# Kernel optimization log

Hardware: AMD Instinct MI355X
Metric: run time of the kernel (lower is better)

Reference implementation:

```python
import jax, jax.numpy as jnp
import numpy as np

B, N, D, H, E, FF = 4, 256, 256, 8, 32, 512
DK = D // H
SCALE = DK ** -0.5
NEG = -9.0e15


def _norm_mul(t, w, b, ms):
    # graph norm over node axis (dim=1)
    mean = jnp.mean(t, axis=1, keepdims=True)
    std = jnp.sqrt(jnp.mean((t - ms * mean) ** 2, axis=1, keepdims=True))
    return w * (t - ms * mean) / (std + 1e-6) + b


def _layer_norm(t, w, b):
    mu = jnp.mean(t, axis=-1, keepdims=True)
    var = jnp.mean((t - mu) ** 2, axis=-1, keepdims=True)
    return w * (t - mu) * jax.lax.rsqrt(var + 1e-5) + b


def _ffn(t, W1, b1, W2, b2):
    return jax.nn.gelu(t @ W1 + b1, approximate=False) @ W2 + b2


def _forward(x, edge_fea, attn_bias, params, adj, adj1, use_adj):
    (gn1_w, gn1_b, gn1_ms, ln1_w, ln1_b, Wq, bq, Wk, bk, Wv, bv,
     Wap, bap, Wep, bep, Wo, bo, Woe, gn2_w, gn2_b, gn2_ms,
     W1, b1, W2, b2, ln2_w, ln2_b, W1e, b1e, W2e, b2e) = params
    adj_f = adj.astype(x.dtype)
    adj1_f = adj1.astype(x.dtype)

    y = _norm_mul(x, gn1_w, gn1_b, gn1_ms)              # [B,N,D]
    e_n = _layer_norm(edge_fea, ln1_w, ln1_b)           # [B,N,N,E]

    q = (y @ Wq + bq).reshape(B, N, H, DK) * SCALE
    k = (y @ Wk + bk).reshape(B, N, H, DK)
    v = (y @ Wv + bv).reshape(B, N, H, DK)
    scores = jnp.einsum('bihd,bjhd->bhij', q, k)        # [B,H,N,N]
    if use_adj:
        scores = jnp.where(adj_f[:, None] > 0, scores, NEG) * adj_f[:, None]

    # global branch: multiplicative attn_bias then softmax
    x_long = jax.nn.softmax(scores * attn_bias, axis=-1)
    out_long = jnp.einsum('bhij,bjhd->bihd', x_long, v)

    # edge-feature fusion
    edge_bias = jnp.swapaxes(e_n @ Wep + bep, 1, 3)     # [B,H,N,N]
    x_proj = (jnp.swapaxes(scores, 1, 3) @ Wap + bap) * adj1_f[..., None]  # [B,N,N,E]
    e_attn = (e_n + x_proj) @ Woe                       # [B,N,N,E]

    # local branch: scores gated by edge bias and local adjacency
    x_local = jax.nn.softmax(scores * edge_bias * adj1_f[:, None], axis=-1)
    out_local = jnp.einsum('bhij,bjhd->bihd', x_local, v)

    attn_out = (out_local + out_long).reshape(B, N, D) @ Wo + bo

    x_out = x + attn_out
    x_out = x_out + _ffn(_norm_mul(x_out, gn2_w, gn2_b, gn2_ms), W1, b1, W2, b2)

    e1 = edge_fea + e_attn
    e_out = e1 + _ffn(_layer_norm(e1, ln2_w, ln2_b), W1e, b1e, W2e, b2e)
    return x_out, e_out


def setup_inputs() -> dict:
    key = jax.random.key(0)
    keys = list(jax.random.split(key, 32))

    def nk():
        return keys.pop()

    def w(shape, s=0.02):
        return jax.random.normal(nk(), shape, jnp.float32) * s

    inp = {}
    inp['x'] = jax.random.normal(nk(), (B, N, D), jnp.float32)
    inp['adj'] = jax.random.randint(nk(), (B, N, N), 0, 2).astype(jnp.int32)
    inp['adj1'] = (jax.random.uniform(nk(), (B, N, N)) < 0.15).astype(jnp.int32)
    inp['use_adj'] = 1
    inp['edge_fea'] = jax.random.normal(nk(), (B, N, N, E), jnp.float32)
    inp['attn_bias'] = jax.random.uniform(nk(), (B, H, N, N), jnp.float32)
    for nm, dim in [('gn1', D), ('gn2', D)]:
        inp[nm + '_w'] = jnp.ones((dim,), jnp.float32)
        inp[nm + '_b'] = jnp.zeros((dim,), jnp.float32)
        inp[nm + '_ms'] = jnp.ones((dim,), jnp.float32)
    for nm, dim in [('ln1', E), ('ln2', E)]:
        inp[nm + '_w'] = jnp.ones((dim,), jnp.float32)
        inp[nm + '_b'] = jnp.zeros((dim,), jnp.float32)
    inp['Wq'], inp['bq'] = w((D, D)), jnp.zeros((D,), jnp.float32)
    inp['Wk'], inp['bk'] = w((D, D)), jnp.zeros((D,), jnp.float32)
    inp['Wv'], inp['bv'] = w((D, D)), jnp.zeros((D,), jnp.float32)
    inp['Wap'], inp['bap'] = w((H, E)), jnp.zeros((E,), jnp.float32)
    inp['Wep'], inp['bep'] = w((E, H)), jnp.zeros((H,), jnp.float32)
    inp['Wo'], inp['bo'] = w((D, D)), jnp.zeros((D,), jnp.float32)
    inp['Woe'] = w((E, E))
    inp['W1'], inp['b1'] = w((D, FF)), jnp.zeros((FF,), jnp.float32)
    inp['W2'], inp['b2'] = w((FF, D)), jnp.zeros((D,), jnp.float32)
    inp['W1e'], inp['b1e'] = w((E, FF)), jnp.zeros((FF,), jnp.float32)
    inp['W2e'], inp['b2e'] = w((FF, E)), jnp.zeros((E,), jnp.float32)
    return inp


def reference(x, adj, adj1, use_adj, edge_fea, attn_bias,
              gn1_w, gn1_b, gn1_ms, gn2_w, gn2_b, gn2_ms,
              ln1_w, ln1_b, ln2_w, ln2_b,
              Wq, bq, Wk, bk, Wv, bv, Wap, bap, Wep, bep, Wo, bo, Woe,
              W1, b1, W2, b2, W1e, b1e, W2e, b2e):
    params = (gn1_w, gn1_b, gn1_ms, ln1_w, ln1_b, Wq, bq, Wk, bk, Wv, bv,
              Wap, bap, Wep, bep, Wo, bo, Woe, gn2_w, gn2_b, gn2_ms,
              W1, b1, W2, b2, ln2_w, ln2_b, W1e, b1e, W2e, b2e)
    return _forward(x, edge_fea, attn_bias, params, adj, adj1, use_adj)
```

## Files before the change

kernel.cpp:

```cpp
#include <hip/hip_runtime.h>
#include <math.h>

constexpr int B_ = 4, N_ = 256, D_ = 256, H_ = 8, E_ = 32, FF_ = 512, DK_ = 32;
constexpr float SCALE_ = 0.17677669529663687f;
constexpr float NEG_ = -9.0e15f;

typedef unsigned short u16;
typedef unsigned int u32;
typedef __attribute__((ext_vector_type(8))) short bf16x8;
typedef __attribute__((ext_vector_type(4))) float f32x4;
typedef __attribute__((ext_vector_type(8))) _Float16 f16x8;
typedef __attribute__((ext_vector_type(2))) _Float16 f16x2;
typedef __attribute__((ext_vector_type(2))) __fp16 fp16x2_raw;

__device__ __forceinline__ float gelu_fast(float x) {
  float u = x * x;
  float q = x * fmaf(-0.071354816272f, u, -1.5957691216057308f);
  float e = __expf(q);
  return x * __builtin_amdgcn_rcpf(1.f + e);
}

__device__ __forceinline__ f16x2 cvt_pk_f16(float a, float b) {
  union { fp16x2_raw i; f16x2 o; } u;
  u.i = __builtin_amdgcn_cvt_pkrtz(a, b);
// ... 288 lines not shown
    if (GELU) v = gelu_fast(v);
    if (res) v += res[(size_t)row * Nn + col];
    C[(size_t)row * Nn + col] = v;
  }
}

__global__ __launch_bounds__(256) void qkv_mfma_kernel(
    const float* __restrict__ A, const u16* __restrict__ wxp,
    const float* __restrict__ bq, const float* __restrict__ bk,
    const float* __restrict__ bv,
    float* __restrict__ q, float* __restrict__ k, float* __restrict__ v) {
  int z = blockIdx.z;
  const u16* Wp = wxp + (size_t)z * 65536;
  const float* bias = (z == 0) ? bq : (z == 1) ? bk : bv;
  float* C = (z == 0) ? q : (z == 1) ? k : v;
  float scale = (z == 0) ? SCALE_ : 1.f;
  int tid = threadIdx.x;
  int w = tid >> 6, l = tid & 63;
  int rt = w & 1, cts = (w >> 1) << 1;
  int row0 = blockIdx.y * 32, col0 = blockIdx.x * 64;
  f32x4 acc[2];
#pragma unroll
  for (int c2 = 0; c2 < 2; c2++) {
    float bb = bias[col0 + (cts + c2) * 16 + (l & 15)];
    acc[c2] = (f32x4){bb, bb, bb, bb};
  }
  int arow = row0 + rt * 16 + (l & 15);
  const float* ap = A + (size_t)arow * D_ + ((l >> 4) << 3);
#pragma unroll
  for (int kc = 0; kc < 8; kc++) {
    float4 a0 = *(const float4*)(ap + kc * 32);
    float4 a1 = *(const float4*)(ap + kc * 32 + 4);
    union { bf16x8 v; u32 u[4]; } af;
    af.u[0] = pk2bf(a0.x, a0.y); af.u[1] = pk2bf(a0.z, a0.w);
    af.u[2] = pk2bf(a1.x, a1.y); af.u[3] = pk2bf(a1.z, a1.w);
#pragma unroll
    for (int c2 = 0; c2 < 2; c2++) {
      bf16x8 wf = *(const bf16x8*)(Wp + (((size_t)kc * 16 + (col0 >> 4) + cts + c2) << 9) + (l << 3));
      acc[c2] = __builtin_amdgcn_mfma_f32_16x16x32_bf16(af.v, wf, acc[c2], 0, 0, 0);
    }
  }
#pragma unroll
  for (int c2 = 0; c2 < 2; c2++) {
    int col = col0 + (cts + c2) * 16 + (l & 15);
#pragma unroll
    for (int rr = 0; rr < 4; rr++) {
      int row = row0 + rt * 16 + (l >> 4) * 4 + rr;
      C[(size_t)row * D_ + col] = acc[c2][rr] * scale;
    }
  }
}

__global__ __launch_bounds__(256) void scores_attn_kernel(
    const float* __restrict__ q, const float* __restrict__ k,
    const float* __restrict__ v, const int* __restrict__ adj,
    const int* __restrict__ use_adj, const float* __restrict__ ab,
    const u16* __restrict__ eb16,
    u16* __restrict__ scoresT, float* __restrict__ out) {
  int it2 = blockIdx.x, h = blockIdx.y, b = blockIdx.z;
  int tid = threadIdx.x;
  __shared__ float qt[16][33];
  __shared__ u16 sc[16][260];
  __shared__ float vst[32][260];
  __shared__ float psw[4][256];

  float kreg[32];
  {
    const float4* kp = (const float4*)(k + ((size_t)b * N_ + tid) * D_ + h * DK_);
#pragma unroll
    for (int i = 0; i < 8; i++) {
      float4 kv = kp[i];
      kreg[4 * i] = kv.x; kreg[4 * i + 1] = kv.y;
      kreg[4 * i + 2] = kv.z; kreg[4 * i + 3] = kv.w;
    }
  }
  for (int i2 = 0; i2 < 2; i2++) {
    int f = tid + (i2 << 8);
    int rr = f >> 5, d = f & 31;
    qt[rr][d] = q[((size_t)b * N_ + it2 * 16 + rr) * D_ + h * DK_ + d];
  }
  for (int i2 = 0; i2 < 32; i2++) {
    int f = tid + (i2 << 8);
    int j = f >> 5, d = f & 31;
    vst[d][j] = v[((size_t)b * N_ + j) * D_ + h * DK_ + d];
  }
  __syncthreads();

  int ua = use_adj[0];
  u32 sbuf[8];
  float sprev = 0.f;
#pragma unroll
  for (int r = 0; r < 16; r++) {
    float s = 0.f;
#pragma unroll
    for (int d = 0; d < 32; d++) s = fmaf(qt[r][d], kreg[d], s);
    int i = it2 * 16 + r;
    if (ua) {
      int a = adj[((size_t)b * N_ + i) * N_ + tid];
      s = (a > 0 ? s : NEG_) * (float)a;
    }
    sc[r][tid] = f2bf(s);
    if (r & 1) sbuf[r >> 1] = pk2bf(sprev, s); else sprev = s;
  }
  uint4* stp = (uint4*)(scoresT + ((((size_t)(b * N_ + tid)) * 8 + h) << 8) + (it2 << 4));
  stp[0] = make_uint4(sbuf[0], sbuf[1], sbuf[2], sbuf[3]);
  stp[1] = make_uint4(sbuf[4], sbuf[5], sbuf[6], sbuf[7]);
  __syncthreads();

  int w = tid >> 6, l = tid & 63;
  int d = l & 31, hf = l >> 5;
  for (int rr = 0; rr < 4; rr++) {
    int lr = w * 4 + rr;
    int i = it2 * 16 + lr;
    size_t base = (((size_t)b * H_ + h) * N_ + i) * N_ + l * 4;
    uint2 sB = *(const uint2*)&sc[lr][l * 4];
    float s4x = bf2f((u16)(sB.x & 0xffff)), s4y = bf2f((u16)(sB.x >> 16));
    float s4z = bf2f((u16)(sB.y & 0xffff)), s4w = bf2f((u16)(sB.y >> 16));
    uint2 eB = *(const uint2*)(eb16 + base);
    float e4x = bf2f((u16)(eB.x & 0xffff)), e4y = bf2f((u16)(eB.x >> 16));
    float e4z = bf2f((u16)(eB.y & 0xffff)), e4w = bf2f((u16)(eB.y >> 16));
    float4 a4 = *(const float4*)(ab + base);
    float sl[4] = {s4x * a4.x, s4y * a4.y, s4z * a4.z, s4w * a4.w};
    float scv[4] = {s4x * e4x, s4y * e4y, s4z * e4z, s4w * e4w};
    float ml = fmaxf(fmaxf(sl[0], sl[1]), fmaxf(sl[2], sl[3]));
    float mc = fmaxf(fmaxf(scv[0], scv[1]), fmaxf(scv[2], scv[3]));
#pragma unroll
    for (int o = 32; o; o >>= 1) { ml = fmaxf(ml, __shfl_xor(ml, o)); mc = fmaxf(mc, __shfl_xor(mc, o)); }
    float el[4], ec[4];
#pragma unroll
    for (int c = 0; c < 4; c++) { el[c] = __expf(sl[c] - ml); ec[c] = __expf(scv[c] - mc); }
    float suml = el[0] + el[1] + el[2] + el[3];
    float sumc = ec[0] + ec[1] + ec[2] + ec[3];
#pragma unroll
    for (int o = 32; o; o >>= 1) { suml += __shfl_xor(suml, o); sumc += __shfl_xor(sumc, o); }
    float rl = __builtin_amdgcn_rcpf(suml), rc = __builtin_amdgcn_rcpf(sumc);
    float4 p;
    p.x = el[0] * rl + ec[0] * rc; p.y = el[1] * rl + ec[1] * rc;
    p.z = el[2] * rl + ec[2] * rc; p.w = el[3] * rl + ec[3] * rc;
    *(float4*)&psw[w][l * 4] = p;
    float acc = 0.f;
#pragma unroll
    for (int jq = 0; jq < 32; jq++) {
      int j4 = hf * 128 + jq * 4;
      float4 pp = *(const float4*)&psw[w][j4];
      float4 vv = *(const float4*)&vst[d][j4];
      acc = fmaf(pp.x, vv.x, acc); acc = fmaf(pp.y, vv.y, acc);
      acc = fmaf(pp.z, vv.z, acc); acc = fmaf(pp.w, vv.w, acc);
    }
    acc += __shfl_xor(acc, 32);
    if (l < 32) out[((size_t)b * N_ + i) * D_ + h * DK_ + d] = acc;
  }
}

__global__ __launch_bounds__(256) void e_fused_kernel(
    const u16* __restrict__ e_nb, const u16* __restrict__ scoresT,
    const int* __restrict__ adj1, const u16* __restrict__ wwp,
    const float* __restrict__ edge_fea,
    const u16* __restrict__ woep, const float* __restrict__ lw,
    const float* __restrict__ lb, const u16* __restrict__ w1p,
    const float* __restrict__ b1e, const u16* __restrict__ w2p,
    const float* __restrict__ b2e, float* __restrict__ e_out) {
  __shared__ float e1s[4][32][36];
  __shared__ float stats[4][2][32];
  int tid = threadIdx.x;
  int w = tid >> 6, l = tid & 63;
  size_t row0 = (size_t)blockIdx.x * 128 + (size_t)w * 32;
  int kb = (l >> 4) * 8;

  bf16x8 wf0 = *(const bf16x8*)(woep + l * 8);
  bf16x8 wf1 = *(const bf16x8*)(woep + 512 + l * 8);
  bf16x8 wwf0 = *(const bf16x8*)(wwp + l * 8);
  bf16x8 wwf1 = *(const bf16x8*)(wwp + 512 + l * 8);
  f32x4 zero = (f32x4){0.f, 0.f, 0.f, 0.f};
  f32x4 eo[2][2];
#pragma unroll
  for (int rt = 0; rt < 2; rt++) {
    size_t gr = row0 + rt * 16 + (l & 15);
    int a1 = adj1[gr];
    bf16x8 enf = *(const bf16x8*)(e_nb + gr * 32 + kb);
    bf16x8 sf = (bf16x8){0, 0, 0, 0, 0, 0, 0, 0};
    int kg = l >> 4;
    if (kg == 0) {
      const u16* sp = scoresT + ((size_t)(gr >> 8) * 8) * 256 + (gr & 255);
#pragma unroll
      for (int hh = 0; hh < 8; hh++)
        sf[hh] = a1 ? (short)sp[hh * 256] : (short)0;
    } else if (kg == 1) {
      sf[0] = a1 ? (short)0x3F80 : (short)0;
    }
    f32x4 acc0 = __builtin_amdgcn_mfma_f32_16x16x32_bf16(sf, wwf0, zero, 0, 0, 0);
    f32x4 acc1 = __builtin_amdgcn_mfma_f32_16x16x32_bf16(sf, wwf1, zero, 0, 0, 0);
    eo[rt][0] = __builtin_amdgcn_mfma_f32_16x16x32_bf16(enf, wf0, acc0, 0, 0, 0);
    eo[rt][1] = __builtin_amdgcn_mfma_f32_16x16x32_bf16(enf, wf1, acc1, 0, 0, 0);
  }
#pragma unroll
  for (int rt = 0; rt < 2; rt++)
#pragma unroll
    for (int ct = 0; ct < 2; ct++) {
      int col = ct * 16 + (l & 15);
#pragma unroll
      for (int rr = 0; rr < 4; rr++) {
        int row = rt * 16 + (l >> 4) * 4 + rr;
        float ed = edge_fea[(row0 + row) * E_ + col];
        e1s[w][row][col] = ed + eo[rt][ct][rr];
      }
    }

  {
    int r = l >> 1, ch = (l & 1) * 16;
    float4 v0 = *(const float4*)&e1s[w][r][ch + 0];
    float4 v1 = *(const float4*)&e1s[w][r][ch + 4];
    float4 v2 = *(const float4*)&e1s[w][r][ch + 8];
    float4 v3 = *(const float4*)&e1s[w][r][ch + 12];
    float s = v0.x + v0.y + v0.z + v0.w + v1.x + v1.y + v1.z + v1.w +
              v2.x + v2.y + v2.z + v2.w + v3.x + v3.y + v3.z + v3.w;
    s += __shfl_xor(s, 1);
    float mu = s * (1.f / E_);
    float tmp[16] = {v0.x, v0.y, v0.z, v0.w, v1.x, v1.y, v1.z, v1.w,
                     v2.x, v2.y, v2.z, v2.w, v3.x, v3.y, v3.z, v3.w};
    float q = 0.f;
#pragma unroll
    for (int i = 0; i < 16; i++) { float dd = tmp[i] - mu; q += dd * dd; }
    q += __shfl_xor(q, 1);
    float inv = rsqrtf(q * (1.f / E_) + 1e-5f);
    stats[w][0][r] = mu;
    stats[w][1][r] = inv;
  }

  bf16x8 at[2];
  {
    float4 lw0 = *(const float4*)(lw + kb), lw1 = *(const float4*)(lw + kb + 4);
    float4 lb0 = *(const float4*)(lb + kb), lb1 = *(const float4*)(lb + kb + 4);
    float lwv[8] = {lw0.x, lw0.y, lw0.z, lw0.w, lw1.x, lw1.y, lw1.z, lw1.w};
    float lbv[8] = {lb0.x, lb0.y, lb0.z, lb0.w, lb1.x, lb1.y, lb1.z, lb1.w};
#pragma unroll
    for (int rt = 0; rt < 2; rt++) {
      int ar = rt * 16 + (l & 15);
      float mu = stats[w][0][ar], inv = stats[w][1][ar];
      float4 e0 = *(const float4*)&e1s[w][ar][kb];
      float4 e1v = *(const float4*)&e1s[w][ar][kb + 4];
      float ev[8] = {e0.x, e0.y, e0.z, e0.w, e1v.x, e1v.y, e1v.z, e1v.w};
#pragma unroll
      for (int j = 0; j < 8; j++)
        at[rt][j] = (short)f2bf(lwv[j] * (ev[j] - mu) * inv + lbv[j]);
    }
  }

  f32x4 oacc[2][2];
#pragma unroll
  for (int ct = 0; ct < 2; ct++) {
    float bb = b2e[ct * 16 + (l & 15)];
#pragma unroll
    for (int rt = 0; rt < 2; rt++)
      oacc[rt][ct] = (f32x4){bb, bb, bb, bb};
  }

#pragma unroll 4
  for (int st = 0; st < 16; st++) {
    bf16x8 w1f0 = *(const bf16x8*)(w1p + (((size_t)st * 2 + 0) << 9) + (l << 3));
    bf16x8 w1f1 = *(const bf16x8*)(w1p + (((size_t)st * 2 + 1) << 9) + (l << 3));
    f16x8 w2f0 = *(const f16x8*)(w2p + (((size_t)st * 2 + 0) << 9) + (l << 3));
    f16x8 w2f1 = *(const f16x8*)(w2p + (((size_t)st * 2 + 1) << 9) + (l << 3));
    float4 b40 = *(const float4*)(b1e + st * 32 + ((l >> 4) << 2));
    float4 b41 = *(const float4*)(b1e + st * 32 + 16 + ((l >> 4) << 2));
    f32x4 hi0 = (f32x4){b40.x, b40.y, b40.z, b40.w};
    f32x4 hi1 = (f32x4){b41.x, b41.y, b41.z, b41.w};
    f32x4 ht00 = __builtin_amdgcn_mfma_f32_16x16x32_bf16(w1f0, at[0], hi0, 0, 0, 0);
    f32x4 ht01 = __builtin_amdgcn_mfma_f32_16x16x32_bf16(w1f0, at[1], hi0, 0, 0, 0);
    f32x4 ht10 = __builtin_amdgcn_mfma_f32_16x16x32_bf16(w1f1, at[0], hi1, 0, 0, 0);
    f32x4 ht11 = __builtin_amdgcn_mfma_f32_16x16x32_bf16(w1f1, at[1], hi1, 0, 0, 0);
    {
      union { f16x8 v; f16x2 h2[4]; } a8;
      a8.h2[0] = gelu_pk(cvt_pk_f16(ht00[0], ht00[1]));
      a8.h2[1] = gelu_pk(cvt_pk_f16(ht00[2], ht00[3]));
      a8.h2[2] = gelu_pk(cvt_pk_f16(ht10[0], ht10[1]));
      a8.h2[3] = gelu_pk(cvt_pk_f16(ht10[2], ht10[3]));
      oacc[0][0] = __builtin_amdgcn_mfma_f32_16x16x32_f16(a8.v, w2f0, oacc[0][0], 0, 0, 0);
      oacc[0][1] = __builtin_amdgcn_mfma_f32_16x16x32_f16(a8.v, w2f1, oacc[0][1], 0, 0, 0);
    }
    {
      union { f16x8 v; f16x2 h2[4]; } a8;
      a8.h2[0] = gelu_pk(cvt_pk_f16(ht01[0], ht01[1]));
      a8.h2[1] = gelu_pk(cvt_pk_f16(ht01[2], ht01[3]));
      a8.h2[2] = gelu_pk(cvt_pk_f16(ht11[0], ht11[1]));
      a8.h2[3] = gelu_pk(cvt_pk_f16(ht11[2], ht11[3]));
      oacc[1][0] = __builtin_amdgcn_mfma_f32_16x16x32_f16(a8.v, w2f0, oacc[1][0], 0, 0, 0);
      oacc[1][1] = __builtin_amdgcn_mfma_f32_16x16x32_f16(a8.v, w2f1, oacc[1][1], 0, 0, 0);
    }
  }

#pragma unroll
  for (int rt = 0; rt < 2; rt++)
#pragma unroll
    for (int ct = 0; ct < 2; ct++) {
      int col = ct * 16 + (l & 15);
#pragma unroll
      for (int r = 0; r < 4; r++) {
        int rl = rt * 16 + (l >> 4) * 4 + r;
        e_out[(row0 + rl) * E_ + col] = e1s[w][rl][col] + oacc[rt][ct][r];
      }
    }
}

extern "C" void kernel_launch(void* const* d_in, const int* in_sizes, int n_in,
                              void* d_out, int out_size, void* d_ws, size_t ws_size,
                              hipStream_t stream) {
  (void)in_sizes; (void)n_in; (void)out_size; (void)ws_size;
  const float* x        = (const float*)d_in[0];
  const int*   adj      = (const int*)d_in[1];
  const int*   adj1     = (const int*)d_in[2];
  const int*   use_adj  = (const int*)d_in[3];
  const float* edge_fea = (const float*)d_in[4];
  const float* attnb    = (const float*)d_in[5];
  const float* gn1_w = (const float*)d_in[6];
  const float* gn1_b = (const float*)d_in[7];
  const float* gn1_ms = (const float*)d_in[8];
  const float* gn2_w = (const float*)d_in[9];
  const float* gn2_b = (const float*)d_in[10];
  const float* gn2_ms = (const float*)d_in[11];
  const float* ln1_w = (const float*)d_in[12];
  const float* ln1_b = (const float*)d_in[13];
  const float* ln2_w = (const float*)d_in[14];
  const float* ln2_b = (const float*)d_in[15];
  const float* Wq = (const float*)d_in[16];
  const float* bq = (const float*)d_in[17];
  const float* Wk = (const float*)d_in[18];
  const float* bk = (const float*)d_in[19];
  const float* Wv = (const float*)d_in[20];
  const float* bv = (const float*)d_in[21];
  const float* Wap = (const float*)d_in[22];
  const float* bap = (const float*)d_in[23];
  const float* Wep = (const float*)d_in[24];
  const float* bep = (const float*)d_in[25];
  const float* Wo = (const float*)d_in[26];
  const float* bo = (const float*)d_in[27];
  const float* Woe = (const float*)d_in[28];
  const float* W1 = (const float*)d_in[29];
  const float* b1 = (const float*)d_in[30];
  const float* W2 = (const float*)d_in[31];
  const float* b2 = (const float*)d_in[32];
  const float* W1e = (const float*)d_in[33];
  const float* b1e = (const float*)d_in[34];
  const float* W2e = (const float*)d_in[35];
  const float* b2e = (const float*)d_in[36];

  float* ws = (float*)d_ws;
  float* y      = ws;
  float* q      = ws + 262144;
  float* k      = ws + 524288;
  float* v      = ws + 786432;
  float* outs   = ws + 1048576;
  float* x_t    = ws + 1310720;
  float* h1     = ws + 1572864;
  u16*   eb16   = (u16*)(ws + 4194304);
  u16*   e_nb   = (u16*)(ws + 6291456);
  u16*   scoresT= (u16*)(ws + 10485760);
  u16*   wbase  = (u16*)(ws + 11534336);
  u16*   w1p    = wbase;
  u16*   w2p    = wbase + 16384;
  u16*   woep   = wbase + 32768;
  u16*   wwp    = wbase + 33792;
  float2* gpart = (float2*)(ws + 11551744);
  u16*   wxp    = (u16*)(ws + 11568128);
  float* x_out  = (float*)d_out;
  float* e_out  = (float*)d_out + 262144;

  dim3 gN(B_, 4, 8);
  front_kernel<<<1472, 256, 0, stream>>>(Wq, Wk, Wv, Wo, W1, W2,
                                         W1e, W2e, Woe, Wap, bap,
                                         wxp, w1p, w2p, woep, wwp,
                                         x, gpart,
                                         edge_fea, ln1_w, ln1_b, Wep, bep, adj1,
                                         e_nb, eb16);
  gnorm_apply_kernel<<<gN, 256, 0, stream>>>(x, gn1_w, gn1_b, gn1_ms, gpart, y);
  qkv_mfma_kernel<<<dim3(4, 32, 3), 256, 0, stream>>>(y, wxp, bq, bk, bv, q, k, v);
  scores_attn_kernel<<<dim3(16, 8, 4), 256, 0, stream>>>(q, k, v, adj, use_adj,
                                                         attnb, eb16, scoresT, outs);
  mgemm32_kernel<0><<<dim3(8, 32), 256, 0, stream>>>(outs, wxp + 196608, bo, x, x_t, 256, 256, 1.f);
  gnorm_part_kernel<<<gN, 256, 0, stream>>>(x_t, gpart);
  gnorm_apply_kernel<<<gN, 256, 0, stream>>>(x_t, gn2_w, gn2_b, gn2_ms, gpart, y);
  mgemm_kernel<1><<<dim3(8, 32), 256, 0, stream>>>(y, wxp + 262144, b1, nullptr, h1, 256, 512, 1.f);
  mgemm32_kernel<0><<<dim3(8, 32), 256, 0, stream>>>(h1, wxp + 393216, b2, x_t, x_out, 512, 256, 1.f);
  e_fused_kernel<<<2048, 256, 0, stream>>>(e_nb, scoresT, adj1, wwp, edge_fea,
                                           woep, ln2_w, ln2_b, w1p, b1e, w2p, b2e, e_out);
}
```

Before: 112.0 us.

## Split edge FFN hidden dimension across two wave groups with LDS reduction

The fused edge kernel now launches 512 threads per block. The first four waves compute the edge-attention residual and layer-norm stats as before. All eight waves then each compute half of the 512-wide FFN hidden dimension, and the partial outputs are combined through shared memory before the final store. This doubles the waves working on the FFN stage to raise parallelism and latency hiding, at the cost of two block-wide barriers, extra LDS and idle waves during the first stage.

```diff
diff --git a/kernel.cpp b/kernel.cpp
--- a/kernel.cpp
+++ b/kernel.cpp
@@ -464,7 +464,7 @@
   }
 }
 
-__global__ __launch_bounds__(256) void e_fused_kernel(
+__global__ __launch_bounds__(512) void e_fused_kernel(
     const u16* __restrict__ e_nb, const u16* __restrict__ scoresT,
     const int* __restrict__ adj1, const u16* __restrict__ wwp,
     const float* __restrict__ edge_fea,
@@ -474,70 +474,74 @@
     const float* __restrict__ b2e, float* __restrict__ e_out) {
   __shared__ float e1s[4][32][36];
   __shared__ float stats[4][2][32];
+  __shared__ float opart[4][32][32];
   int tid = threadIdx.x;
   int w = tid >> 6, l = tid & 63;
-  size_t row0 = (size_t)blockIdx.x * 128 + (size_t)w * 32;
+  int wg = w & 3, half = w >> 2;
+  size_t row0 = (size_t)blockIdx.x * 128 + (size_t)wg * 32;
   int kb = (l >> 4) * 8;
 
-  bf16x8 wf0 = *(const bf16x8*)(woep + l * 8);
-  bf16x8 wf1 = *(const bf16x8*)(woep + 512 + l * 8);
-  bf16x8 wwf0 = *(const bf16x8*)(wwp + l * 8);
-  bf16x8 wwf1 = *(const bf16x8*)(wwp + 512 + l * 8);
-  f32x4 zero = (f32x4){0.f, 0.f, 0.f, 0.f};
-  f32x4 eo[2][2];
-#pragma unroll
-  for (int rt = 0; rt < 2; rt++) {
-    size_t gr = row0 + rt * 16 + (l & 15);
-    int a1 = adj1[gr];
-    bf16x8 enf = *(const bf16x8*)(e_nb + gr * 32 + kb);
-    bf16x8 sf = (bf16x8){0, 0, 0, 0, 0, 0, 0, 0};
-    int kg = l >> 4;
-    if (kg == 0) {
-      const u16* sp = scoresT + ((size_t)(gr >> 8) * 8) * 256 + (gr & 255);
-#pragma unroll
-      for (int hh = 0; hh < 8; hh++)
-        sf[hh] = a1 ? (short)sp[hh * 256] : (short)0;
-    } else if (kg == 1) {
-      sf[0] = a1 ? (short)0x3F80 : (short)0;
-    }
-    f32x4 acc0 = __builtin_amdgcn_mfma_f32_16x16x32_bf16(sf, wwf0, zero, 0, 0, 0);
-    f32x4 acc1 = __builtin_amdgcn_mfma_f32_16x16x32_bf16(sf, wwf1, zero, 0, 0, 0);
-    eo[rt][0] = __builtin_amdgcn_mfma_f32_16x16x32_bf16(enf, wf0, acc0, 0, 0, 0);
-    eo[rt][1] = __builtin_amdgcn_mfma_f32_16x16x32_bf16(enf, wf1, acc1, 0, 0, 0);
-  }
-#pragma unroll
-  for (int rt = 0; rt < 2; rt++)
-#pragma unroll
-    for (int ct = 0; ct < 2; ct++) {
-      int col = ct * 16 + (l & 15);
-#pragma unroll
-      for (int rr = 0; rr < 4; rr++) {
-        int row = rt * 16 + (l >> 4) * 4 + rr;
-        float ed = edge_fea[(row0 + row) * E_ + col];
-        e1s[w][row][col] = ed + eo[rt][ct][rr];
+  if (half == 0) {
+    bf16x8 wf0 = *(const bf16x8*)(woep + l * 8);
+    bf16x8 wf1 = *(const bf16x8*)(woep + 512 + l * 8);
+    bf16x8 wwf0 = *(const bf16x8*)(wwp + l * 8);
+    bf16x8 wwf1 = *(const bf16x8*)(wwp + 512 + l * 8);
+    f32x4 zero = (f32x4){0.f, 0.f, 0.f, 0.f};
+    f32x4 eo[2][2];
+#pragma unroll
+    for (int rt = 0; rt < 2; rt++) {
+      size_t gr = row0 + rt * 16 + (l & 15);
+      int a1 = adj1[gr];
+      bf16x8 enf = *(const bf16x8*)(e_nb + gr * 32 + kb);
+      bf16x8 sf = (bf16x8){0, 0, 0, 0, 0, 0, 0, 0};
+      int kg = l >> 4;
+      if (kg == 0) {
+        const u16* sp = scoresT + ((size_t)(gr >> 8) * 8) * 256 + (gr & 255);
+#pragma unroll
+        for (int hh = 0; hh < 8; hh++)
+          sf[hh] = a1 ? (short)sp[hh * 256] : (short)0;
+      } else if (kg == 1) {
+        sf[0] = a1 ? (short)0x3F80 : (short)0;
       }
-    }
-
-  {
-    int r = l >> 1, ch = (l & 1) * 16;
-    float4 v0 = *(const float4*)&e1s[w][r][ch + 0];
-    float4 v1 = *(const float4*)&e1s[w][r][ch + 4];
-    float4 v2 = *(const float4*)&e1s[w][r][ch + 8];
-    float4 v3 = *(const float4*)&e1s[w][r][ch + 12];
-    float s = v0.x + v0.y + v0.z + v0.w + v1.x + v1.y + v1.z + v1.w +
-              v2.x + v2.y + v2.z + v2.w + v3.x + v3.y + v3.z + v3.w;
-    s += __shfl_xor(s, 1);
-    float mu = s * (1.f / E_);
-    float tmp[16] = {v0.x, v0.y, v0.z, v0.w, v1.x, v1.y, v1.z, v1.w,
-                     v2.x, v2.y, v2.z, v2.w, v3.x, v3.y, v3.z, v3.w};
-    float q = 0.f;
-#pragma unroll
-    for (int i = 0; i < 16; i++) { float dd = tmp[i] - mu; q += dd * dd; }
-    q += __shfl_xor(q, 1);
-    float inv = rsqrtf(q * (1.f / E_) + 1e-5f);
-    stats[w][0][r] = mu;
-    stats[w][1][r] = inv;
-  }
+      f32x4 acc0 = __builtin_amdgcn_mfma_f32_16x16x32_bf16(sf, wwf0, zero, 0, 0, 0);
+      f32x4 acc1 = __builtin_amdgcn_mfma_f32_16x16x32_bf16(sf, wwf1, zero, 0, 0, 0);
+      eo[rt][0] = __builtin_amdgcn_mfma_f32_16x16x32_bf16(enf, wf0, acc0, 0, 0, 0);
+      eo[rt][1] = __builtin_amdgcn_mfma_f32_16x16x32_bf16(enf, wf1, acc1, 0, 0, 0);
+    }
+#pragma unroll
+    for (int rt = 0; rt < 2; rt++)
+#pragma unroll
+      for (int ct = 0; ct < 2; ct++) {
+        int col = ct * 16 + (l & 15);
+#pragma unroll
+        for (int rr = 0; rr < 4; rr++) {
+          int row = rt * 16 + (l >> 4) * 4 + rr;
+          float ed = edge_fea[(row0 + row) * E_ + col];
+          e1s[wg][row][col] = ed + eo[rt][ct][rr];
+        }
+      }
+    {
+      int r = l >> 1, ch = (l & 1) * 16;
+      float4 v0 = *(const float4*)&e1s[wg][r][ch + 0];
+      float4 v1 = *(const float4*)&e1s[wg][r][ch + 4];
+      float4 v2 = *(const float4*)&e1s[wg][r][ch + 8];
+      float4 v3 = *(const float4*)&e1s[wg][r][ch + 12];
+      float s = v0.x + v0.y + v0.z + v0.w + v1.x + v1.y + v1.z + v1.w +
+                v2.x + v2.y + v2.z + v2.w + v3.x + v3.y + v3.z + v3.w;
+      s += __shfl_xor(s, 1);
+      float mu = s * (1.f / E_);
+      float tmp[16] = {v0.x, v0.y, v0.z, v0.w, v1.x, v1.y, v1.z, v1.w,
+                       v2.x, v2.y, v2.z, v2.w, v3.x, v3.y, v3.z, v3.w};
+      float q = 0.f;
+#pragma unroll
+      for (int i = 0; i < 16; i++) { float dd = tmp[i] - mu; q += dd * dd; }
+      q += __shfl_xor(q, 1);
+      float inv = rsqrtf(q * (1.f / E_) + 1e-5f);
+      stats[wg][0][r] = mu;
+      stats[wg][1][r] = inv;
+    }
+  }
+  __syncthreads();
 
   bf16x8 at[2];
   {
@@ -548,9 +552,9 @@
 #pragma unroll
     for (int rt = 0; rt < 2; rt++) {
       int ar = rt * 16 + (l & 15);
-      float mu = stats[w][0][ar], inv = stats[w][1][ar];
-      float4 e0 = *(const float4*)&e1s[w][ar][kb];
-      float4 e1v = *(const float4*)&e1s[w][ar][kb + 4];
+      float mu = stats[wg][0][ar], inv = stats[wg][1][ar];
+      float4 e0 = *(const float4*)&e1s[wg][ar][kb];
+      float4 e1v = *(const float4*)&e1s[wg][ar][kb + 4];
       float ev[8] = {e0.x, e0.y, e0.z, e0.w, e1v.x, e1v.y, e1v.z, e1v.w};
 #pragma unroll
       for (int j = 0; j < 8; j++)
@@ -561,14 +565,16 @@
   f32x4 oacc[2][2];
 #pragma unroll
   for (int ct = 0; ct < 2; ct++) {
-    float bb = b2e[ct * 16 + (l & 15)];
+    float bb = half == 0 ? b2e[ct * 16 + (l & 15)] : 0.f;
 #pragma unroll
     for (int rt = 0; rt < 2; rt++)
       oacc[rt][ct] = (f32x4){bb, bb, bb, bb};
   }
 
+  int st0 = half * 8;
 #pragma unroll 4
-  for (int st = 0; st < 16; st++) {
+  for (int si = 0; si < 8; si++) {
+    int st = st0 + si;
     bf16x8 w1f0 = *(const bf16x8*)(w1p + (((size_t)st * 2 + 0) << 9) + (l << 3));
     bf16x8 w1f1 = *(const bf16x8*)(w1p + (((size_t)st * 2 + 1) << 9) + (l << 3));
     f16x8 w2f0 = *(const f16x8*)(w2p + (((size_t)st * 2 + 0) << 9) + (l << 3));
@@ -601,17 +607,34 @@
     }
   }
 
-#pragma unroll
-  for (int rt = 0; rt < 2; rt++)
-#pragma unroll
-    for (int ct = 0; ct < 2; ct++) {
-      int col = ct * 16 + (l & 15);
-#pragma unroll
-      for (int r = 0; r < 4; r++) {
-        int rl = rt * 16 + (l >> 4) * 4 + r;
-        e_out[(row0 + rl) * E_ + col] = e1s[w][rl][col] + oacc[rt][ct][r];
+  if (half == 1) {
+#pragma unroll
+    for (int rt = 0; rt < 2; rt++)
+#pragma unroll
+      for (int ct = 0; ct < 2; ct++) {
+        int col = ct * 16 + (l & 15);
+#pragma unroll
+        for (int r = 0; r < 4; r++) {
+          int rl = rt * 16 + (l >> 4) * 4 + r;
+          opart[wg][rl][col] = oacc[rt][ct][r];
+        }
       }
-    }
+  }
+  __syncthreads();
+  if (half == 0) {
+#pragma unroll
+    for (int rt = 0; rt < 2; rt++)
+#pragma unroll
+      for (int ct = 0; ct < 2; ct++) {
+        int col = ct * 16 + (l & 15);
+#pragma unroll
+        for (int r = 0; r < 4; r++) {
+          int rl = rt * 16 + (l >> 4) * 4 + r;
+          e_out[(row0 + rl) * E_ + col] =
+              e1s[wg][rl][col] + oacc[rt][ct][r] + opart[wg][rl][col];
+        }
+      }
+  }
 }
 
 extern "C" void kernel_launch(void* const* d_in, const int* in_sizes, int n_in,
@@ -693,6 +716,6 @@
   gnorm_apply_kernel<<<gN, 256, 0, stream>>>(x_t, gn2_w, gn2_b, gn2_ms, gpart, y);
   mgemm_kernel<1><<<dim3(8, 32), 256, 0, stream>>>(y, wxp + 262144, b1, nullptr, h1, 256, 512, 1.f);
   mgemm32_kernel<0><<<dim3(8, 32), 256, 0, stream>>>(h1, wxp + 393216, b2, x_t, x_out, 512, 256, 1.f);
-  e_fused_kernel<<<2048, 256, 0, stream>>>(e_nb, scoresT, adj1, wwp, edge_fea,
+  e_fused_kernel<<<2048, 512, 0, stream>>>(e_nb, scoresT, adj1, wwp, edge_fea,
                                            woep, ln2_w, ln2_b, w1p, b1e, w2p, b2e, e_out);
 }
```

New measurement: 115.1 us. +2.7%, slower.

## Stage edge FFN weights in LDS and double block size in e_fused_kernel

Applied to the files above, without the earlier changes.

The edge FFN kernel now copies the full W1e/W2e packed weights and b1e bias into shared memory once per block, instead of each wave reading them from global memory inside the hidden-dimension loop. Blocks grow to 512 threads covering 256 rows, which halves the grid and spreads each weight copy over more rows. The cost is about 104 KB of dynamic LDS per block, which limits how many blocks fit on a CU, plus an extra barrier and an upfront copy before compute can start.

```diff
diff --git a/kernel.cpp b/kernel.cpp
--- a/kernel.cpp
+++ b/kernel.cpp
@@ -464,7 +464,7 @@
   }
 }
 
-__global__ __launch_bounds__(256) void e_fused_kernel(
+__global__ __launch_bounds__(512, 2) void e_fused_kernel(
     const u16* __restrict__ e_nb, const u16* __restrict__ scoresT,
     const int* __restrict__ adj1, const u16* __restrict__ wwp,
     const float* __restrict__ edge_fea,
@@ -472,12 +472,27 @@
     const float* __restrict__ lb, const u16* __restrict__ w1p,
     const float* __restrict__ b1e, const u16* __restrict__ w2p,
     const float* __restrict__ b2e, float* __restrict__ e_out) {
-  __shared__ float e1s[4][32][36];
-  __shared__ float stats[4][2][32];
+  extern __shared__ __align__(16) char smem[];
+  u16* w1s = (u16*)smem;
+  u16* w2s = (u16*)(smem + 32768);
+  float* b1s = (float*)(smem + 65536);
+  float (*e1s)[32][36] = (float(*)[32][36])(smem + 67584);
+  float (*stats)[2][32] = (float(*)[2][32])(smem + 67584 + 36864);
+
   int tid = threadIdx.x;
   int w = tid >> 6, l = tid & 63;
-  size_t row0 = (size_t)blockIdx.x * 128 + (size_t)w * 32;
+  size_t row0 = (size_t)blockIdx.x * 256 + (size_t)w * 32;
   int kb = (l >> 4) * 8;
+
+  {
+    uint4* d1 = (uint4*)w1s; const uint4* g1 = (const uint4*)w1p;
+    uint4* d2 = (uint4*)w2s; const uint4* g2 = (const uint4*)w2p;
+#pragma unroll
+    for (int i = 0; i < 4; i++) d1[tid + 512 * i] = g1[tid + 512 * i];
+#pragma unroll
+    for (int i = 0; i < 4; i++) d2[tid + 512 * i] = g2[tid + 512 * i];
+    b1s[tid] = b1e[tid];
+  }
 
   bf16x8 wf0 = *(const bf16x8*)(woep + l * 8);
   bf16x8 wf1 = *(const bf16x8*)(woep + 512 + l * 8);
@@ -539,6 +554,8 @@
     stats[w][1][r] = inv;
   }
 
+  __syncthreads();
+
   bf16x8 at[2];
   {
     float4 lw0 = *(const float4*)(lw + kb), lw1 = *(const float4*)(lw + kb + 4);
@@ -567,14 +584,15 @@
       oacc[rt][ct] = (f32x4){bb, bb, bb, bb};
   }
 
+  int lsh = l << 3, brow = (l >> 4) << 2;
 #pragma unroll 4
   for (int st = 0; st < 16; st++) {
-    bf16x8 w1f0 = *(const bf16x8*)(w1p + (((size_t)st * 2 + 0) << 9) + (l << 3));
-    bf16x8 w1f1 = *(const bf16x8*)(w1p + (((size_t)st * 2 + 1) << 9) + (l << 3));
-    f16x8 w2f0 = *(const f16x8*)(w2p + (((size_t)st * 2 + 0) << 9) + (l << 3));
-    f16x8 w2f1 = *(const f16x8*)(w2p + (((size_t)st * 2 + 1) << 9) + (l << 3));
-    float4 b40 = *(const float4*)(b1e + st * 32 + ((l >> 4) << 2));
-    float4 b41 = *(const float4*)(b1e + st * 32 + 16 + ((l >> 4) << 2));
+    bf16x8 w1f0 = *(const bf16x8*)(w1s + ((st * 2 + 0) << 9) + lsh);
+    bf16x8 w1f1 = *(const bf16x8*)(w1s + ((st * 2 + 1) << 9) + lsh);
+    f16x8 w2f0 = *(const f16x8*)(w2s + ((st * 2 + 0) << 9) + lsh);
+    f16x8 w2f1 = *(const f16x8*)(w2s + ((st * 2 + 1) << 9) + lsh);
+    float4 b40 = *(const float4*)(b1s + st * 32 + brow);
+    float4 b41 = *(const float4*)(b1s + st * 32 + 16 + brow);
     f32x4 hi0 = (f32x4){b40.x, b40.y, b40.z, b40.w};
     f32x4 hi1 = (f32x4){b41.x, b41.y, b41.z, b41.w};
     f32x4 ht00 = __builtin_amdgcn_mfma_f32_16x16x32_bf16(w1f0, at[0], hi0, 0, 0, 0);
@@ -693,6 +711,6 @@
   gnorm_apply_kernel<<<gN, 256, 0, stream>>>(x_t, gn2_w, gn2_b, gn2_ms, gpart, y);
   mgemm_kernel<1><<<dim3(8, 32), 256, 0, stream>>>(y, wxp + 262144, b1, nullptr, h1, 256, 512, 1.f);
   mgemm32_kernel<0><<<dim3(8, 32), 256, 0, stream>>>(h1, wxp + 393216, b2, x_t, x_out, 512, 256, 1.f);
-  e_fused_kernel<<<2048, 256, 0, stream>>>(e_nb, scoresT, adj1, wwp, edge_fea,
-                                           woep, ln2_w, ln2_b, w1p, b1e, w2p, b2e, e_out);
-}
+  e_fused_kernel<<<1024, 512, 106496, stream>>>(e_nb, scoresT, adj1, wwp, edge_fea,
+                                                woep, ln2_w, ln2_b, w1p, b1e, w2p, b2e, e_out);
+}
```

New measurement: 115.4 us. 3.0% more time.

## Make edge FFN kernel persistent over four tiles with register prefetch of next tile

Applied to the files above, without the earlier changes.

The fused edge kernel now processes four 128-row tiles per block, with a quarter as many blocks launched. Each iteration software-prefetches the next tile's adj1, e_nb, scores and edge_fea values into registers while computing the current one. Weight fragments and LayerNorm parameters are loaded once per block and reused across tiles. The aim is to hide global load latency and amortise per-block setup, at the cost of extra register pressure (lower occupancy) and less parallelism from fewer blocks.

```diff
diff --git a/kernel.cpp b/kernel.cpp
--- a/kernel.cpp
+++ b/kernel.cpp
@@ -464,6 +464,35 @@
   }
 }
 
+__device__ __forceinline__ void tile_load(
+    size_t rowb, int l, int kb,
+    const int* __restrict__ adj1, const u16* __restrict__ e_nb,
+    const u16* __restrict__ scoresT, const float* __restrict__ edge_fea,
+    int a1[2], bf16x8 enf[2], u16 sg[2][8], float ed[16]) {
+#pragma unroll
+  for (int rt = 0; rt < 2; rt++) {
+    size_t gr = rowb + rt * 16 + (l & 15);
+    a1[rt] = adj1[gr];
+    enf[rt] = *(const bf16x8*)(e_nb + gr * 32 + kb);
+    if ((l >> 4) == 0) {
+      const u16* sp = scoresT + ((size_t)(gr >> 8) * 8) * 256 + (gr & 255);
+#pragma unroll
+      for (int hh = 0; hh < 8; hh++) sg[rt][hh] = sp[hh * 256];
+    }
+  }
+#pragma unroll
+  for (int rt = 0; rt < 2; rt++)
+#pragma unroll
+    for (int ct = 0; ct < 2; ct++) {
+      int col = ct * 16 + (l & 15);
+#pragma unroll
+      for (int rr = 0; rr < 4; rr++) {
+        int row = rt * 16 + (l >> 4) * 4 + rr;
+        ed[(rt * 2 + ct) * 4 + rr] = edge_fea[(rowb + row) * E_ + col];
+      }
+    }
+}
+
 __global__ __launch_bounds__(256) void e_fused_kernel(
     const u16* __restrict__ e_nb, const u16* __restrict__ scoresT,
     const int* __restrict__ adj1, const u16* __restrict__ wwp,
@@ -476,75 +505,89 @@
   __shared__ float stats[4][2][32];
   int tid = threadIdx.x;
   int w = tid >> 6, l = tid & 63;
-  size_t row0 = (size_t)blockIdx.x * 128 + (size_t)w * 32;
   int kb = (l >> 4) * 8;
 
   bf16x8 wf0 = *(const bf16x8*)(woep + l * 8);
   bf16x8 wf1 = *(const bf16x8*)(woep + 512 + l * 8);
   bf16x8 wwf0 = *(const bf16x8*)(wwp + l * 8);
   bf16x8 wwf1 = *(const bf16x8*)(wwp + 512 + l * 8);
-  f32x4 zero = (f32x4){0.f, 0.f, 0.f, 0.f};
-  f32x4 eo[2][2];
-#pragma unroll
-  for (int rt = 0; rt < 2; rt++) {
-    size_t gr = row0 + rt * 16 + (l & 15);
-    int a1 = adj1[gr];
-    bf16x8 enf = *(const bf16x8*)(e_nb + gr * 32 + kb);
-    bf16x8 sf = (bf16x8){0, 0, 0, 0, 0, 0, 0, 0};
-    int kg = l >> 4;
-    if (kg == 0) {
-      const u16* sp = scoresT + ((size_t)(gr >> 8) * 8) * 256 + (gr & 255);
-#pragma unroll
-      for (int hh = 0; hh < 8; hh++)
-        sf[hh] = a1 ? (short)sp[hh * 256] : (short)0;
-    } else if (kg == 1) {
-      sf[0] = a1 ? (short)0x3F80 : (short)0;
-    }
-    f32x4 acc0 = __builtin_amdgcn_mfma_f32_16x16x32_bf16(sf, wwf0, zero, 0, 0, 0);
-    f32x4 acc1 = __builtin_amdgcn_mfma_f32_16x16x32_bf16(sf, wwf1, zero, 0, 0, 0);
-    eo[rt][0] = __builtin_amdgcn_mfma_f32_16x16x32_bf16(enf, wf0, acc0, 0, 0, 0);
-    eo[rt][1] = __builtin_amdgcn_mfma_f32_16x16x32_bf16(enf, wf1, acc1, 0, 0, 0);
-  }
-#pragma unroll
-  for (int rt = 0; rt < 2; rt++)
-#pragma unroll
-    for (int ct = 0; ct < 2; ct++) {
-      int col = ct * 16 + (l & 15);
-#pragma unroll
-      for (int rr = 0; rr < 4; rr++) {
-        int row = rt * 16 + (l >> 4) * 4 + rr;
-        float ed = edge_fea[(row0 + row) * E_ + col];
-        e1s[w][row][col] = ed + eo[rt][ct][rr];
-      }
-    }
-
-  {
-    int r = l >> 1, ch = (l & 1) * 16;
-    float4 v0 = *(const float4*)&e1s[w][r][ch + 0];
-    float4 v1 = *(const float4*)&e1s[w][r][ch + 4];
-    float4 v2 = *(const float4*)&e1s[w][r][ch + 8];
-    float4 v3 = *(const float4*)&e1s[w][r][ch + 12];
-    float s = v0.x + v0.y + v0.z + v0.w + v1.x + v1.y + v1.z + v1.w +
-              v2.x + v2.y + v2.z + v2.w + v3.x + v3.y + v3.z + v3.w;
-    s += __shfl_xor(s, 1);
-    float mu = s * (1.f / E_);
-    float tmp[16] = {v0.x, v0.y, v0.z, v0.w, v1.x, v1.y, v1.z, v1.w,
-                     v2.x, v2.y, v2.z, v2.w, v3.x, v3.y, v3.z, v3.w};
-    float q = 0.f;
-#pragma unroll
-    for (int i = 0; i < 16; i++) { float dd = tmp[i] - mu; q += dd * dd; }
-    q += __shfl_xor(q, 1);
-    float inv = rsqrtf(q * (1.f / E_) + 1e-5f);
-    stats[w][0][r] = mu;
-    stats[w][1][r] = inv;
-  }
-
-  bf16x8 at[2];
+  float lwv[8], lbv[8];
   {
     float4 lw0 = *(const float4*)(lw + kb), lw1 = *(const float4*)(lw + kb + 4);
     float4 lb0 = *(const float4*)(lb + kb), lb1 = *(const float4*)(lb + kb + 4);
-    float lwv[8] = {lw0.x, lw0.y, lw0.z, lw0.w, lw1.x, lw1.y, lw1.z, lw1.w};
-    float lbv[8] = {lb0.x, lb0.y, lb0.z, lb0.w, lb1.x, lb1.y, lb1.z, lb1.w};
+    lwv[0] = lw0.x; lwv[1] = lw0.y; lwv[2] = lw0.z; lwv[3] = lw0.w;
+    lwv[4] = lw1.x; lwv[5] = lw1.y; lwv[6] = lw1.z; lwv[7] = lw1.w;
+    lbv[0] = lb0.x; lbv[1] = lb0.y; lbv[2] = lb0.z; lbv[3] = lb0.w;
+    lbv[4] = lb1.x; lbv[5] = lb1.y; lbv[6] = lb1.z; lbv[7] = lb1.w;
+  }
+  float bb2[2] = {b2e[(l & 15)], b2e[16 + (l & 15)]};
+
+  int a1c[2]; bf16x8 enfc[2]; u16 sgc[2][8]; float edc[16];
+  int a1n[2]; bf16x8 enfn[2]; u16 sgn[2][8]; float edn[16];
+
+  size_t tbase = (size_t)blockIdx.x * 4;
+  tile_load(tbase * 128 + (size_t)w * 32, l, kb, adj1, e_nb, scoresT, edge_fea,
+            a1c, enfc, sgc, edc);
+
+#pragma unroll
+  for (int it = 0; it < 4; it++) {
+    size_t rowb = (tbase + it) * 128 + (size_t)w * 32;
+    if (it < 3)
+      tile_load((tbase + it + 1) * 128 + (size_t)w * 32, l, kb,
+                adj1, e_nb, scoresT, edge_fea, a1n, enfn, sgn, edn);
+
+    f32x4 zero = (f32x4){0.f, 0.f, 0.f, 0.f};
+    f32x4 eo[2][2];
+#pragma unroll
+    for (int rt = 0; rt < 2; rt++) {
+      bf16x8 sf = (bf16x8){0, 0, 0, 0, 0, 0, 0, 0};
+      int kg = l >> 4;
+      if (kg == 0) {
+#pragma unroll
+        for (int hh = 0; hh < 8; hh++)
+          sf[hh] = a1c[rt] ? (short)sgc[rt][hh] : (short)0;
+      } else if (kg == 1) {
+        sf[0] = a1c[rt] ? (short)0x3F80 : (short)0;
+      }
+      f32x4 acc0 = __builtin_amdgcn_mfma_f32_16x16x32_bf16(sf, wwf0, zero, 0, 0, 0);
+      f32x4 acc1 = __builtin_amdgcn_mfma_f32_16x16x32_bf16(sf, wwf1, zero, 0, 0, 0);
+      eo[rt][0] = __builtin_amdgcn_mfma_f32_16x16x32_bf16(enfc[rt], wf0, acc0, 0, 0, 0);
+      eo[rt][1] = __builtin_amdgcn_mfma_f32_16x16x32_bf16(enfc[rt], wf1, acc1, 0, 0, 0);
+    }
+#pragma unroll
+    for (int rt = 0; rt < 2; rt++)
+#pragma unroll
+      for (int ct = 0; ct < 2; ct++) {
+        int col = ct * 16 + (l & 15);
+#pragma unroll
+        for (int rr = 0; rr < 4; rr++) {
+          int row = rt * 16 + (l >> 4) * 4 + rr;
+          e1s[w][row][col] = edc[(rt * 2 + ct) * 4 + rr] + eo[rt][ct][rr];
+        }
+      }
+
+    {
+      int r = l >> 1, ch = (l & 1) * 16;
+      float4 v0 = *(const float4*)&e1s[w][r][ch + 0];
+      float4 v1 = *(const float4*)&e1s[w][r][ch + 4];
+      float4 v2 = *(const float4*)&e1s[w][r][ch + 8];
+      float4 v3 = *(const float4*)&e1s[w][r][ch + 12];
+      float s = v0.x + v0.y + v0.z + v0.w + v1.x + v1.y + v1.z + v1.w +
+                v2.x + v2.y + v2.z + v2.w + v3.x + v3.y + v3.z + v3.w;
+      s += __shfl_xor(s, 1);
+      float mu = s * (1.f / E_);
+      float tmp[16] = {v0.x, v0.y, v0.z, v0.w, v1.x, v1.y, v1.z, v1.w,
+                       v2.x, v2.y, v2.z, v2.w, v3.x, v3.y, v3.z, v3.w};
+      float q = 0.f;
+#pragma unroll
+      for (int i = 0; i < 16; i++) { float dd = tmp[i] - mu; q += dd * dd; }
+      q += __shfl_xor(q, 1);
+      float inv = rsqrtf(q * (1.f / E_) + 1e-5f);
+      stats[w][0][r] = mu;
+      stats[w][1][r] = inv;
+    }
+
+    bf16x8 at[2];
 #pragma unroll
     for (int rt = 0; rt < 2; rt++) {
       int ar = rt * 16 + (l & 15);
@@ -556,62 +599,71 @@
       for (int j = 0; j < 8; j++)
         at[rt][j] = (short)f2bf(lwv[j] * (ev[j] - mu) * inv + lbv[j]);
     }
-  }
-
-  f32x4 oacc[2][2];
-#pragma unroll
-  for (int ct = 0; ct < 2; ct++) {
-    float bb = b2e[ct * 16 + (l & 15)];
+
+    f32x4 oacc[2][2];
+#pragma unroll
+    for (int ct = 0; ct < 2; ct++) {
+      float bb = bb2[ct];
+#pragma unroll
+      for (int rt = 0; rt < 2; rt++)
+        oacc[rt][ct] = (f32x4){bb, bb, bb, bb};
+    }
+
+#pragma unroll 4
+    for (int st = 0; st < 16; st++) {
+      bf16x8 w1f0 = *(const bf16x8*)(w1p + (((size_t)st * 2 + 0) << 9) + (l << 3));
+      bf16x8 w1f1 = *(const bf16x8*)(w1p + (((size_t)st * 2 + 1) << 9) + (l << 3));
+      f16x8 w2f0 = *(const f16x8*)(w2p + (((size_t)st * 2 + 0) << 9) + (l << 3));
+      f16x8 w2f1 = *(const f16x8*)(w2p + (((size_t)st * 2 + 1) << 9) + (l << 3));
+      float4 b40 = *(const float4*)(b1e + st * 32 + ((l >> 4) << 2));
+      float4 b41 = *(const float4*)(b1e + st * 32 + 16 + ((l >> 4) << 2));
+      f32x4 hi0 = (f32x4){b40.x, b40.y, b40.z, b40.w};
+      f32x4 hi1 = (f32x4){b41.x, b41.y, b41.z, b41.w};
+      f32x4 ht00 = __builtin_amdgcn_mfma_f32_16x16x32_bf16(w1f0, at[0], hi0, 0, 0, 0);
+      f32x4 ht01 = __builtin_amdgcn_mfma_f32_16x16x32_bf16(w1f0, at[1], hi0, 0, 0, 0);
+      f32x4 ht10 = __builtin_amdgcn_mfma_f32_16x16x32_bf16(w1f1, at[0], hi1, 0, 0, 0);
+      f32x4 ht11 = __builtin_amdgcn_mfma_f32_16x16x32_bf16(w1f1, at[1], hi1, 0, 0, 0);
+      {
+        union { f16x8 v; f16x2 h2[4]; } a8;
+        a8.h2[0] = gelu_pk(cvt_pk_f16(ht00[0], ht00[1]));
+        a8.h2[1] = gelu_pk(cvt_pk_f16(ht00[2], ht00[3]));
+        a8.h2[2] = gelu_pk(cvt_pk_f16(ht10[0], ht10[1]));
+        a8.h2[3] = gelu_pk(cvt_pk_f16(ht10[2], ht10[3]));
+        oacc[0][0] = __builtin_amdgcn_mfma_f32_16x16x32_f16(a8.v, w2f0, oacc[0][0], 0, 0, 0);
+        oacc[0][1] = __builtin_amdgcn_mfma_f32_16x16x32_f16(a8.v, w2f1, oacc[0][1], 0, 0, 0);
+      }
+      {
+        union { f16x8 v; f16x2 h2[4]; } a8;
+        a8.h2[0] = gelu_pk(cvt_pk_f16(ht01[0], ht01[1]));
+        a8.h2[1] = gelu_pk(cvt_pk_f16(ht01[2], ht01[3]));
+        a8.h2[2] = gelu_pk(cvt_pk_f16(ht11[0], ht11[1]));
+        a8.h2[3] = gelu_pk(cvt_pk_f16(ht11[2], ht11[3]));
+        oacc[1][0] = __builtin_amdgcn_mfma_f32_16x16x32_f16(a8.v, w2f0, oacc[1][0], 0, 0, 0);
+        oacc[1][1] = __builtin_amdgcn_mfma_f32_16x16x32_f16(a8.v, w2f1, oacc[1][1], 0, 0, 0);
+      }
+    }
+
 #pragma unroll
     for (int rt = 0; rt < 2; rt++)
-      oacc[rt][ct] = (f32x4){bb, bb, bb, bb};
-  }
-
-#pragma unroll 4
-  for (int st = 0; st < 16; st++) {
-    bf16x8 w1f0 = *(const bf16x8*)(w1p + (((size_t)st * 2 + 0) << 9) + (l << 3));
-    bf16x8 w1f1 = *(const bf16x8*)(w1p + (((size_t)st * 2 + 1) << 9) + (l << 3));
-    f16x8 w2f0 = *(const f16x8*)(w2p + (((size_t)st * 2 + 0) << 9) + (l << 3));
-    f16x8 w2f1 = *(const f16x8*)(w2p + (((size_t)st * 2 + 1) << 9) + (l << 3));
-    float4 b40 = *(const float4*)(b1e + st * 32 + ((l >> 4) << 2));
-    float4 b41 = *(const float4*)(b1e + st * 32 + 16 + ((l >> 4) << 2));
-    f32x4 hi0 = (f32x4){b40.x, b40.y, b40.z, b40.w};
-    f32x4 hi1 = (f32x4){b41.x, b41.y, b41.z, b41.w};
-    f32x4 ht00 = __builtin_amdgcn_mfma_f32_16x16x32_bf16(w1f0, at[0], hi0, 0, 0, 0);
-    f32x4 ht01 = __builtin_amdgcn_mfma_f32_16x16x32_bf16(w1f0, at[1], hi0, 0, 0, 0);
-    f32x4 ht10 = __builtin_amdgcn_mfma_f32_16x16x32_bf16(w1f1, at[0], hi1, 0, 0, 0);
-    f32x4 ht11 = __builtin_amdgcn_mfma_f32_16x16x32_bf16(w1f1, at[1], hi1, 0, 0, 0);
-    {
-      union { f16x8 v; f16x2 h2[4]; } a8;
-      a8.h2[0] = gelu_pk(cvt_pk_f16(ht00[0], ht00[1]));
-      a8.h2[1] = gelu_pk(cvt_pk_f16(ht00[2], ht00[3]));
-      a8.h2[2] = gelu_pk(cvt_pk_f16(ht10[0], ht10[1]));
-      a8.h2[3] = gelu_pk(cvt_pk_f16(ht10[2], ht10[3]));
-      oacc[0][0] = __builtin_amdgcn_mfma_f32_16x16x32_f16(a8.v, w2f0, oacc[0][0], 0, 0, 0);
-      oacc[0][1] = __builtin_amdgcn_mfma_f32_16x16x32_f16(a8.v, w2f1, oacc[0][1], 0, 0, 0);
-    }
-    {
-      union { f16x8 v; f16x2 h2[4]; } a8;
-      a8.h2[0] = gelu_pk(cvt_pk_f16(ht01[0], ht01[1]));
-      a8.h2[1] = gelu_pk(cvt_pk_f16(ht01[2], ht01[3]));
-      a8.h2[2] = gelu_pk(cvt_pk_f16(ht11[0], ht11[1]));
-      a8.h2[3] = gelu_pk(cvt_pk_f16(ht11[2], ht11[3]));
-      oacc[1][0] = __builtin_amdgcn_mfma_f32_16x16x32_f16(a8.v, w2f0, oacc[1][0], 0, 0, 0);
-      oacc[1][1] = __builtin_amdgcn_mfma_f32_16x16x32_f16(a8.v, w2f1, oacc[1][1], 0, 0, 0);
-    }
-  }
-
-#pragma unroll
-  for (int rt = 0; rt < 2; rt++)
-#pragma unroll
-    for (int ct = 0; ct < 2; ct++) {
-      int col = ct * 16 + (l & 15);
-#pragma unroll
-      for (int r = 0; r < 4; r++) {
-        int rl = rt * 16 + (l >> 4) * 4 + r;
-        e_out[(row0 + rl) * E_ + col] = e1s[w][rl][col] + oacc[rt][ct][r];
+#pragma unroll
+      for (int ct = 0; ct < 2; ct++) {
+        int col = ct * 16 + (l & 15);
+#pragma unroll
+        for (int r = 0; r < 4; r++) {
+          int rl = rt * 16 + (l >> 4) * 4 + r;
+          e_out[(rowb + rl) * E_ + col] = e1s[w][rl][col] + oacc[rt][ct][r];
+        }
       }
-    }
+
+    if (it < 3) {
+      a1c[0] = a1n[0]; a1c[1] = a1n[1];
+      enfc[0] = enfn[0]; enfc[1] = enfn[1];
+#pragma unroll
+      for (int j = 0; j < 8; j++) { sgc[0][j] = sgn[0][j]; sgc[1][j] = sgn[1][j]; }
+#pragma unroll
+      for (int j = 0; j < 16; j++) edc[j] = edn[j];
+    }
+  }
 }
 
 extern "C" void kernel_launch(void* const* d_in, const int* in_sizes, int n_in,
@@ -693,6 +745,6 @@
   gnorm_apply_kernel<<<gN, 256, 0, stream>>>(x_t, gn2_w, gn2_b, gn2_ms, gpart, y);
   mgemm_kernel<1><<<dim3(8, 32), 256, 0, stream>>>(y, wxp + 262144, b1, nullptr, h1, 256, 512, 1.f);
   mgemm32_kernel<0><<<dim3(8, 32), 256, 0, stream>>>(h1, wxp + 393216, b2, x_t, x_out, 512, 256, 1.f);
-  e_fused_kernel<<<2048, 256, 0, stream>>>(e_nb, scoresT, adj1, wwp, edge_fea,
-                                           woep, ln2_w, ln2_b, w1p, b1e, w2p, b2e, e_out);
-}
+  e_fused_kernel<<<512, 256, 0, stream>>>(e_nb, scoresT, adj1, wwp, edge_fea,
+                                          woep, ln2_w, ln2_b, w1p, b1e, w2p, b2e, e_out);
+}
```

New measurement: 120.5 us. 7.5% more time.
